# Performance work log

Measured on AMD Instinct MI355X. Metric: run time of the kernel, lower is better.

Reference implementation:

```python
import jax, jax.numpy as jnp
import numpy as np

B, S = 16, 32768
LEVELS = (5, 20)
TIME_DIM = 8
NUM_FREQS = 6  # frequency xyz encoder: 3*(1+2*6)=39 dims
HID = 128
IN_DIM = 3 * (1 + 2 * NUM_FREQS) + 2 * TIME_DIM  # 55


def setup_inputs() -> dict:
    key = jax.random.key(0)
    ks = jax.random.split(key, 16)
    time = jax.random.uniform(ks[0], (B,), dtype=jnp.float32)
    xyz = jax.random.uniform(ks[1], (B, S, 3), dtype=jnp.float32) * 2.0 - 1.0  # in [-1,1]
    te0 = jax.random.normal(ks[2], (LEVELS[0] + 1, TIME_DIM), dtype=jnp.float32)
    te1 = jax.random.normal(ks[3], (LEVELS[1] + 1, TIME_DIM), dtype=jnp.float32)
    W0 = jax.random.normal(ks[4], (IN_DIM, HID), dtype=jnp.float32) * 0.05
    b0 = jnp.zeros((HID,), dtype=jnp.float32)
    W1 = jax.random.normal(ks[5], (HID, HID), dtype=jnp.float32) * 0.05
    b1 = jnp.zeros((HID,), dtype=jnp.float32)
    W2 = jax.random.normal(ks[6], (HID, HID), dtype=jnp.float32) * 0.05
    b2 = jnp.zeros((HID,), dtype=jnp.float32)
    Wout = jax.random.normal(ks[7], (HID, 1), dtype=jnp.float32) * 0.05
    bout = jnp.zeros((1,), dtype=jnp.float32)
    return {"time": time, "xyz": xyz, "te0": te0, "te1": te1,
            "W0": W0, "b0": b0, "W1": W1, "b1": b1, "W2": W2, "b2": b2,
            "Wout": Wout, "bout": bout}


def _time_encode(t, emb, L):
    # bucketize t into L uniform intervals on [0,1), lerp between bucket endpoints
    tL = t * L
    idx = jnp.clip(jnp.floor(tL).astype(jnp.int32), 0, L - 1)  # (B,)
    w = (idx + 1).astype(t.dtype) - tL                          # weight for lower endpoint
    lerped = w[:, None] * emb[idx] + (1.0 - w)[:, None] * emb[idx + 1]
    # t >= 1: use last embedding directly (torch fallback branch)
    return jnp.where((t >= 1.0)[:, None], emb[L][None, :], lerped)


def _xyz_encode(x):
    # frequency encoding, include_input, freqs 2^0..2^(NUM_FREQS-1)
    freqs = jnp.asarray(2.0 ** np.arange(NUM_FREQS), dtype=x.dtype)  # (F,)
    xp = x[:, None, :] * freqs[None, :, None]                         # (N, F, 3)
    n = x.shape[0]
    return jnp.concatenate([x, jnp.sin(xp).reshape(n, -1), jnp.cos(xp).reshape(n, -1)], axis=-1)


def reference(time, xyz, te0, te1, W0, b0, W1, b1, W2, b2, Wout, bout):
    s = xyz.shape[1]
    t_enc = jnp.concatenate([_time_encode(time, te0, LEVELS[0]),
                             _time_encode(time, te1, LEVELS[1])], axis=-1)  # (B, 16)
    t_enc = jnp.repeat(t_enc, s, axis=0)          # (B*S, 16)  'B d -> (B S) d'
    pts = (xyz.reshape(-1, 3) + 1.0) / 2.0        # (B*S, 3)
    x = jnp.concatenate([t_enc, _xyz_encode(pts)], axis=1)  # (B*S, 55)
    x = jax.nn.relu(x @ W0 + b0)
    x = jax.nn.relu(x @ W1 + b1)
    x = jax.nn.relu(x @ W2 + b2)
    return x @ Wout + bout  # (B*S, 1)
```

## Files before the change

kernel.cpp:

```cpp
#include <hip/hip_runtime.h>

typedef _Float16 f16;
typedef __attribute__((ext_vector_type(2))) __fp16 fp16x2;
typedef __attribute__((ext_vector_type(8))) _Float16 f16x8;
typedef __attribute__((ext_vector_type(4))) float f32x4;
typedef __attribute__((ext_vector_type(4))) unsigned int u32x4;

#define NPTS   (16 * 32768)
#define W0P_OFF 0
#define W1P_OFF (16 * 1024)
#define W2P_OFF (48 * 1024)
#define WOP_OFF (80 * 1024)
#define FRAGS_BYTES (84 * 1024)
#define B0E_OFF FRAGS_BYTES
#define WS_NEEDED (FRAGS_BYTES + 8192)
#define LDS_TOTAL 4096

__global__ void pack_weights(const float* __restrict__ time, const float* __restrict__ te0,
                             const float* __restrict__ te1, const float* __restrict__ W0,
                             const float* __restrict__ b0, const float* __restrict__ W1,
                             const float* __restrict__ W2, const float* __restrict__ Wout,
                             unsigned char* __restrict__ ws) {
  const int bi = blockIdx.x;
  const int l = threadIdx.x;
  const int g = l >> 4, r16 = l & 15;
  if (bi < 84) {
    const float* W; int obase, fi, kt, mt, kmax; bool natural, outcol;
    if (bi < 16)      { W = W0;   fi = bi;      mt = fi >> 1; kt = fi & 1; obase = W0P_OFF; kmax = 39;  natural = true;  outcol = false; }
    else if (bi < 48) { W = W1;   fi = bi - 16; mt = fi >> 2; kt = fi & 3; obase = W1P_OFF; kmax = 128; natural = false; outcol = false; }
    else if (bi < 80) { W = W2;   fi = bi - 48; mt = fi >> 2; kt = fi & 3; obase = W2P_OFF; kmax = 128; natural = false; outcol = false; }
    else              { W = Wout; fi = bi - 80; mt = 0;       kt = fi;     obase = WOP_OFF; kmax = 128; natural = false; outcol = true;  }
    const int m = mt * 16 + r16;
    f16 vals[8] __attribute__((aligned(16)));
#pragma unroll
    for (int j = 0; j < 8; ++j) {
      const int k = natural ? (kt * 32 + g * 8 + j)
                            : (kt * 32 + (j >> 2) * 16 + g * 4 + (j & 3));
      float v = 0.f;
      if (k < kmax) {
        if (outcol)       v = (m == 0) ? Wout[k] : 0.f;
        else if (natural) v = W[(16 + k) * 128 + m];
        else              v = W[k * 128 + m];
      }
      vals[j] = (f16)v;
    }
    *(u32x4*)(ws + obase + (fi * 64 + l) * 16) = *(const u32x4*)vals;
  } else {
    const int idx = (bi - 84) * 64 + l;
    const int b = idx >> 7, m = idx & 127;
    const float t = time[b];
    float acc = b0[m];
#pragma unroll
    for (int d = 0; d < 16; ++d) {
      const float* emb; int L, dd;
      if (d < 8) { emb = te0; L = 5;  dd = d; }
      else       { emb = te1; L = 20; dd = d - 8; }
      const float tL = t * (float)L;
      int i = (int)floorf(tL);
      i = i < 0 ? 0 : (i > L - 1 ? L - 1 : i);
      const float wlo = (float)(i + 1) - tL;
      float v = wlo * emb[i * 8 + dd] + (1.f - wlo) * emb[(i + 1) * 8 + dd];
      if (t >= 1.f) v = emb[L * 8 + dd];
      acc += v * W0[d * 128 + m];
    }
    ((float*)(ws + B0E_OFF))[b * 128 + m] = acc;
  }
}

__device__ __forceinline__ unsigned int pkmax0(unsigned int x) {
  unsigned int r;
  asm("v_pk_max_f16 %0, %1, %2" : "=v"(r) : "v"(x), "v"(0u));
  return r;
}
__device__ __forceinline__ unsigned int pkrtz(float a, float b) {
  union { fp16x2 h; unsigned int u; } c;
  c.h = __builtin_amdgcn_cvt_pkrtz(a, b);
  return c.u;
}
__device__ __forceinline__ float hwsin_rev(float rev) {
  float r; asm("v_sin_f32 %0, %1" : "=v"(r) : "v"(rev)); return r;
}
__device__ __forceinline__ float hwcos_rev(float rev) {
  float r; asm("v_cos_f32 %0, %1" : "=v"(r) : "v"(rev)); return r;
}

template <int KT>
__device__ __forceinline__ void layer_swapped(const unsigned char* __restrict__ wsrc,
                                              const float* __restrict__ bias,
                                              const f16x8 (&Bin)[KT][4], f16x8 (&Bout)[4][4],
                                              int lane) {
  const int g4 = (lane >> 4) * 4;
  f16x8 Ab[2];
  Ab[0] = *(const f16x8*)(wsrc + (0 * 64 + lane) * 16);
#pragma unroll
  for (int mt = 0; mt < 8; ++mt) {
    const float4 bv = *(const float4*)(bias + mt * 16 + g4);
    f32x4 acc[4];
#pragma unroll
    for (int nt = 0; nt < 4; ++nt) acc[nt] = (f32x4){bv.x, bv.y, bv.z, bv.w};
#pragma unroll
    for (int kt = 0; kt < KT; ++kt) {
      const int s = mt * KT + kt;
      if (s + 1 < 8 * KT)
        Ab[(s + 1) & 1] = *(const f16x8*)(wsrc + ((s + 1) * 64 + lane) * 16);
      __builtin_amdgcn_s_setprio(1);
#pragma unroll
      for (int nt = 0; nt < 4; ++nt)
        acc[nt] = __builtin_amdgcn_mfma_f32_16x16x32_f16(Ab[s & 1], Bin[kt][nt], acc[nt], 0, 0, 0);
      __builtin_amdgcn_s_setprio(0);
    }
#pragma unroll
    for (int nt = 0; nt < 4; ++nt) {
      union { f16x8 v; unsigned int w[4]; } ub;
      ub.v = Bout[mt >> 1][nt];
      ub.w[2 * (mt & 1) + 0] = pkmax0(pkrtz(acc[nt][0], acc[nt][1]));
      ub.w[2 * (mt & 1) + 1] = pkmax0(pkrtz(acc[nt][2], acc[nt][3]));
      Bout[mt >> 1][nt] = ub.v;
    }
  }
}

__global__ void __launch_bounds__(64, 1)
mlp_main(const float* __restrict__ xyz, const float* __restrict__ b1,
         const float* __restrict__ b2, const float* __restrict__ bout,
         const unsigned char* __restrict__ ws, float* __restrict__ out) {
  extern __shared__ char lds[];
  const int lane = threadIdx.x;
  const int g = lane >> 4, r16 = lane & 15;

  char* scr = lds;
  const float bo = bout[0];

  const int pbase = blockIdx.x * 64;
  const int p = pbase + lane;

  float ff[40];
  const float xs0 = xyz[p * 3], xs1 = xyz[p * 3 + 1], xs2 = xyz[p * 3 + 2];
  const float pcs[3] = {(xs0 + 1.f) * 0.5f, (xs1 + 1.f) * 0.5f, (xs2 + 1.f) * 0.5f};
  const float INV2PI = 0.15915494309189535f;
#pragma unroll
  for (int c = 0; c < 3; ++c) {
    ff[c] = pcs[c];
    const float rev = pcs[c] * INV2PI;
    float s = hwsin_rev(rev), co = hwcos_rev(rev);
#pragma unroll
    for (int f = 0; f < 6; ++f) {
      ff[3 + f * 3 + c] = s;
      ff[21 + f * 3 + c] = co;
      const float s2 = 2.f * s * co, c2 = 1.f - 2.f * s * s;
      s = s2; co = c2;
    }
  }
  ff[39] = 0.f;
  unsigned int fw[32];
#pragma unroll
  for (int i = 0; i < 20; ++i) fw[i] = pkrtz(ff[2 * i], ff[2 * i + 1]);
#pragma unroll
  for (int i = 20; i < 32; ++i) fw[i] = 0u;

  f16x8 B0[2][4];
#pragma unroll
  for (int h = 0; h < 2; ++h) {
    if ((lane >> 5) == h) {
#pragma unroll
      for (int s = 0; s < 8; ++s)
        *(u32x4*)(scr + (lane & 31) * 128 + ((s ^ (lane & 7)) * 16)) = ((const u32x4*)fw)[s];
    }
    asm volatile("s_waitcnt lgkmcnt(0)" ::: "memory");
#pragma unroll
    for (int kt = 0; kt < 2; ++kt)
#pragma unroll
      for (int nn = 0; nn < 2; ++nn) {
        const int row = nn * 16 + r16;
        B0[kt][h * 2 + nn] = *(const f16x8*)(scr + row * 128 + (((4 * kt + g) ^ (row & 7)) * 16));
      }
    asm volatile("s_waitcnt lgkmcnt(0)" ::: "memory");
  }

  const float* b0e = (const float*)(ws + B0E_OFF) + (blockIdx.x >> 9) * 128;
  f16x8 Bx[4][4], By[4][4];
  layer_swapped<2>(ws + W0P_OFF, b0e, B0, Bx, lane);
  layer_swapped<4>(ws + W1P_OFF, b1, Bx, By, lane);
  layer_swapped<4>(ws + W2P_OFF, b2, By, Bx, lane);

  f16x8 Ob[2];
  Ob[0] = *(const f16x8*)(ws + WOP_OFF + (0 * 64 + lane) * 16);
  const f32x4 bovec = (f32x4){bo, bo, bo, bo};
  f32x4 accO[4];
#pragma unroll
  for (int kt = 0; kt < 4; ++kt) {
    if (kt + 1 < 4)
      Ob[(kt + 1) & 1] = *(const f16x8*)(ws + WOP_OFF + ((kt + 1) * 64 + lane) * 16);
    __builtin_amdgcn_s_setprio(1);
    if (kt == 0) {
#pragma unroll
      for (int nt = 0; nt < 4; ++nt)
        accO[nt] = __builtin_amdgcn_mfma_f32_16x16x32_f16(Ob[0], Bx[0][nt], bovec, 0, 0, 0);
    } else {
#pragma unroll
      for (int nt = 0; nt < 4; ++nt)
        accO[nt] = __builtin_amdgcn_mfma_f32_16x16x32_f16(Ob[kt & 1], Bx[kt][nt], accO[nt], 0, 0, 0);
    }
    __builtin_amdgcn_s_setprio(0);
  }

  const float a0 = __shfl(accO[0][0], r16, 64);
  const float a1 = __shfl(accO[1][0], r16, 64);
  const float a2 = __shfl(accO[2][0], r16, 64);
  const float a3 = __shfl(accO[3][0], r16, 64);
  const float v = g == 0 ? a0 : g == 1 ? a1 : g == 2 ? a2 : a3;
  out[pbase + lane] = v;
}

extern "C" void kernel_launch(void* const* d_in, const int* in_sizes, int n_in,
                              void* d_out, int out_size, void* d_ws, size_t ws_size,
                              hipStream_t stream) {
  const float* time = (const float*)d_in[0];
  const float* xyz  = (const float*)d_in[1];
  const float* te0  = (const float*)d_in[2];
  const float* te1  = (const float*)d_in[3];
  const float* W0   = (const float*)d_in[4];
  const float* b0   = (const float*)d_in[5];
  const float* W1   = (const float*)d_in[6];
  const float* b1   = (const float*)d_in[7];
  const float* W2   = (const float*)d_in[8];
  const float* b2   = (const float*)d_in[9];
  const float* Wout = (const float*)d_in[10];
  const float* bout = (const float*)d_in[11];
  float* out = (float*)d_out;
  unsigned char* ws = (unsigned char*)d_ws;
  if (ws_size < WS_NEEDED) return;

  pack_weights<<<116, 64, 0, stream>>>(time, te0, te1, W0, b0, W1, W2, Wout, ws);
  mlp_main<<<NPTS / 64, 64, LDS_TOTAL, stream>>>(xyz, b1, b2, bout, ws, out);
}
```

Measured before the change: 48.31 us.

## Process 96 points per wave and fold time encoding into layer-0 input

Each single-wave block now handles 96 points (6 N-tiles) instead of 64, so every weight fragment load feeds more MFMAs. The per-batch layer-0 bias folding is replaced by putting the 16 time-encoding features into the first-layer input (K=55 within two K-tiles), which simplifies pack_weights and builds features twice per wave. Launch bounds are relaxed to allow 2 waves per SIMD. The cost is more registers for the wider accumulators and activations, which risks spills or lower occupancy, plus a tail block with clamped indices.

```diff
diff --git a/kernel.cpp b/kernel.cpp
--- a/kernel.cpp
+++ b/kernel.cpp
@@ -7,63 +7,57 @@
 typedef __attribute__((ext_vector_type(4))) unsigned int u32x4;
 
 #define NPTS   (16 * 32768)
+#define PTSPB  96
+#define NBLK   ((NPTS + PTSPB - 1) / PTSPB)
 #define W0P_OFF 0
 #define W1P_OFF (16 * 1024)
 #define W2P_OFF (48 * 1024)
 #define WOP_OFF (80 * 1024)
 #define FRAGS_BYTES (84 * 1024)
-#define B0E_OFF FRAGS_BYTES
-#define WS_NEEDED (FRAGS_BYTES + 8192)
+#define TENC_OFF FRAGS_BYTES
+#define WS_NEEDED (FRAGS_BYTES + 1024)
 #define LDS_TOTAL 4096
 
 __global__ void pack_weights(const float* __restrict__ time, const float* __restrict__ te0,
                              const float* __restrict__ te1, const float* __restrict__ W0,
-                             const float* __restrict__ b0, const float* __restrict__ W1,
-                             const float* __restrict__ W2, const float* __restrict__ Wout,
-                             unsigned char* __restrict__ ws) {
+                             const float* __restrict__ W1, const float* __restrict__ W2,
+                             const float* __restrict__ Wout, unsigned char* __restrict__ ws) {
   const int bi = blockIdx.x;
   const int l = threadIdx.x;
   const int g = l >> 4, r16 = l & 15;
   if (bi < 84) {
     const float* W; int obase, fi, kt, mt, kmax; bool natural, outcol;
-    if (bi < 16)      { W = W0;   fi = bi;      mt = fi >> 1; kt = fi & 1; obase = W0P_OFF; kmax = 39;  natural = true;  outcol = false; }
+    if (bi < 16)      { W = W0;   fi = bi;      mt = fi >> 1; kt = fi & 1; obase = W0P_OFF; kmax = 55;  natural = true;  outcol = false; }
     else if (bi < 48) { W = W1;   fi = bi - 16; mt = fi >> 2; kt = fi & 3; obase = W1P_OFF; kmax = 128; natural = false; outcol = false; }
     else if (bi < 80) { W = W2;   fi = bi - 48; mt = fi >> 2; kt = fi & 3; obase = W2P_OFF; kmax = 128; natural = false; outcol = false; }
     else              { W = Wout; fi = bi - 80; mt = 0;       kt = fi;     obase = WOP_OFF; kmax = 128; natural = false; outcol = true;  }
     const int m = mt * 16 + r16;
+    int KTl = (bi < 16) ? 2 : 4;
+    int si = outcol ? kt : (mt * KTl + kt);
     f16 vals[8] __attribute__((aligned(16)));
 #pragma unroll
     for (int j = 0; j < 8; ++j) {
       const int k = natural ? (kt * 32 + g * 8 + j)
                             : (kt * 32 + (j >> 2) * 16 + g * 4 + (j & 3));
       float v = 0.f;
-      if (k < kmax) {
-        if (outcol)       v = (m == 0) ? Wout[k] : 0.f;
-        else if (natural) v = W[(16 + k) * 128 + m];
-        else              v = W[k * 128 + m];
-      }
+      if (k < kmax) v = outcol ? ((m == 0) ? Wout[k] : 0.f) : W[k * 128 + m];
       vals[j] = (f16)v;
     }
-    *(u32x4*)(ws + obase + (fi * 64 + l) * 16) = *(const u32x4*)vals;
+    *(u32x4*)(ws + obase + (si * 64 + l) * 16) = *(const u32x4*)vals;
   } else {
     const int idx = (bi - 84) * 64 + l;
-    const int b = idx >> 7, m = idx & 127;
+    const int b = idx >> 4, d = idx & 15;
     const float t = time[b];
-    float acc = b0[m];
-#pragma unroll
-    for (int d = 0; d < 16; ++d) {
-      const float* emb; int L, dd;
-      if (d < 8) { emb = te0; L = 5;  dd = d; }
-      else       { emb = te1; L = 20; dd = d - 8; }
-      const float tL = t * (float)L;
-      int i = (int)floorf(tL);
-      i = i < 0 ? 0 : (i > L - 1 ? L - 1 : i);
-      const float wlo = (float)(i + 1) - tL;
-      float v = wlo * emb[i * 8 + dd] + (1.f - wlo) * emb[(i + 1) * 8 + dd];
-      if (t >= 1.f) v = emb[L * 8 + dd];
-      acc += v * W0[d * 128 + m];
-    }
-    ((float*)(ws + B0E_OFF))[b * 128 + m] = acc;
+    const float* emb; int L, dd;
+    if (d < 8) { emb = te0; L = 5;  dd = d; }
+    else       { emb = te1; L = 20; dd = d - 8; }
+    const float tL = t * (float)L;
+    int i = (int)floorf(tL);
+    i = i < 0 ? 0 : (i > L - 1 ? L - 1 : i);
+    const float wlo = (float)(i + 1) - tL;
+    float v = wlo * emb[i * 8 + dd] + (1.f - wlo) * emb[(i + 1) * 8 + dd];
+    if (t >= 1.f) v = emb[L * 8 + dd];
+    ((float*)(ws + TENC_OFF))[idx] = v;
   }
 }
 
@@ -84,10 +78,38 @@
   float r; asm("v_cos_f32 %0, %1" : "=v"(r) : "v"(rev)); return r;
 }
 
+__device__ __forceinline__ void build_feat(const float* __restrict__ xyz,
+                                           const unsigned char* __restrict__ ws,
+                                           int p, unsigned int* fw) {
+  const float* tb = (const float*)(ws + TENC_OFF) + (p >> 15) * 16;
+  float ff[64];
+#pragma unroll
+  for (int i = 0; i < 16; ++i) ff[i] = tb[i];
+  const float xs0 = xyz[p * 3], xs1 = xyz[p * 3 + 1], xs2 = xyz[p * 3 + 2];
+  const float pcs[3] = {(xs0 + 1.f) * 0.5f, (xs1 + 1.f) * 0.5f, (xs2 + 1.f) * 0.5f};
+  const float INV2PI = 0.15915494309189535f;
+#pragma unroll
+  for (int c = 0; c < 3; ++c) {
+    ff[16 + c] = pcs[c];
+    float s = hwsin_rev(pcs[c] * INV2PI), co = hwcos_rev(pcs[c] * INV2PI);
+#pragma unroll
+    for (int f = 0; f < 6; ++f) {
+      ff[19 + f * 3 + c] = s;
+      ff[37 + f * 3 + c] = co;
+      const float s2 = 2.f * s * co, c2 = 1.f - 2.f * s * s;
+      s = s2; co = c2;
+    }
+  }
+#pragma unroll
+  for (int i = 55; i < 64; ++i) ff[i] = 0.f;
+#pragma unroll
+  for (int i = 0; i < 32; ++i) fw[i] = pkrtz(ff[2 * i], ff[2 * i + 1]);
+}
+
 template <int KT>
 __device__ __forceinline__ void layer_swapped(const unsigned char* __restrict__ wsrc,
                                               const float* __restrict__ bias,
-                                              const f16x8 (&Bin)[KT][4], f16x8 (&Bout)[4][4],
+                                              const f16x8 (&Bin)[KT][6], f16x8 (&Bout)[4][6],
                                               int lane) {
   const int g4 = (lane >> 4) * 4;
   f16x8 Ab[2];
@@ -95,9 +117,9 @@
 #pragma unroll
   for (int mt = 0; mt < 8; ++mt) {
     const float4 bv = *(const float4*)(bias + mt * 16 + g4);
-    f32x4 acc[4];
-#pragma unroll
-    for (int nt = 0; nt < 4; ++nt) acc[nt] = (f32x4){bv.x, bv.y, bv.z, bv.w};
+    f32x4 acc[6];
+#pragma unroll
+    for (int nt = 0; nt < 6; ++nt) acc[nt] = (f32x4){bv.x, bv.y, bv.z, bv.w};
 #pragma unroll
     for (int kt = 0; kt < KT; ++kt) {
       const int s = mt * KT + kt;
@@ -105,12 +127,12 @@
         Ab[(s + 1) & 1] = *(const f16x8*)(wsrc + ((s + 1) * 64 + lane) * 16);
       __builtin_amdgcn_s_setprio(1);
 #pragma unroll
-      for (int nt = 0; nt < 4; ++nt)
+      for (int nt = 0; nt < 6; ++nt)
         acc[nt] = __builtin_amdgcn_mfma_f32_16x16x32_f16(Ab[s & 1], Bin[kt][nt], acc[nt], 0, 0, 0);
       __builtin_amdgcn_s_setprio(0);
     }
 #pragma unroll
-    for (int nt = 0; nt < 4; ++nt) {
+    for (int nt = 0; nt < 6; ++nt) {
       union { f16x8 v; unsigned int w[4]; } ub;
       ub.v = Bout[mt >> 1][nt];
       ub.w[2 * (mt & 1) + 0] = pkmax0(pkrtz(acc[nt][0], acc[nt][1]));
@@ -120,45 +142,25 @@
   }
 }
 
-__global__ void __launch_bounds__(64, 1)
-mlp_main(const float* __restrict__ xyz, const float* __restrict__ b1,
-         const float* __restrict__ b2, const float* __restrict__ bout,
-         const unsigned char* __restrict__ ws, float* __restrict__ out) {
+__global__ void __launch_bounds__(64, 2)
+mlp_main(const float* __restrict__ xyz, const float* __restrict__ b0,
+         const float* __restrict__ b1, const float* __restrict__ b2,
+         const float* __restrict__ bout, const unsigned char* __restrict__ ws,
+         float* __restrict__ out) {
   extern __shared__ char lds[];
   const int lane = threadIdx.x;
   const int g = lane >> 4, r16 = lane & 15;
-
   char* scr = lds;
   const float bo = bout[0];
 
-  const int pbase = blockIdx.x * 64;
-  const int p = pbase + lane;
-
-  float ff[40];
-  const float xs0 = xyz[p * 3], xs1 = xyz[p * 3 + 1], xs2 = xyz[p * 3 + 2];
-  const float pcs[3] = {(xs0 + 1.f) * 0.5f, (xs1 + 1.f) * 0.5f, (xs2 + 1.f) * 0.5f};
-  const float INV2PI = 0.15915494309189535f;
-#pragma unroll
-  for (int c = 0; c < 3; ++c) {
-    ff[c] = pcs[c];
-    const float rev = pcs[c] * INV2PI;
-    float s = hwsin_rev(rev), co = hwcos_rev(rev);
-#pragma unroll
-    for (int f = 0; f < 6; ++f) {
-      ff[3 + f * 3 + c] = s;
-      ff[21 + f * 3 + c] = co;
-      const float s2 = 2.f * s * co, c2 = 1.f - 2.f * s * s;
-      s = s2; co = c2;
-    }
-  }
-  ff[39] = 0.f;
+  const int pbase = blockIdx.x * PTSPB;
+
   unsigned int fw[32];
-#pragma unroll
-  for (int i = 0; i < 20; ++i) fw[i] = pkrtz(ff[2 * i], ff[2 * i + 1]);
-#pragma unroll
-  for (int i = 20; i < 32; ++i) fw[i] = 0u;
-
-  f16x8 B0[2][4];
+  {
+    int p = pbase + lane; p = p < NPTS ? p : NPTS - 1;
+    build_feat(xyz, ws, p, fw);
+  }
+  f16x8 B0[2][6];
 #pragma unroll
   for (int h = 0; h < 2; ++h) {
     if ((lane >> 5) == h) {
@@ -176,17 +178,34 @@
       }
     asm volatile("s_waitcnt lgkmcnt(0)" ::: "memory");
   }
-
-  const float* b0e = (const float*)(ws + B0E_OFF) + (blockIdx.x >> 9) * 128;
-  f16x8 Bx[4][4], By[4][4];
-  layer_swapped<2>(ws + W0P_OFF, b0e, B0, Bx, lane);
+  {
+    int p = pbase + 64 + (lane & 31); p = p < NPTS ? p : NPTS - 1;
+    build_feat(xyz, ws, p, fw);
+  }
+  if (lane < 32) {
+#pragma unroll
+    for (int s = 0; s < 8; ++s)
+      *(u32x4*)(scr + (lane & 31) * 128 + ((s ^ (lane & 7)) * 16)) = ((const u32x4*)fw)[s];
+  }
+  asm volatile("s_waitcnt lgkmcnt(0)" ::: "memory");
+#pragma unroll
+  for (int kt = 0; kt < 2; ++kt)
+#pragma unroll
+    for (int nn = 0; nn < 2; ++nn) {
+      const int row = nn * 16 + r16;
+      B0[kt][4 + nn] = *(const f16x8*)(scr + row * 128 + (((4 * kt + g) ^ (row & 7)) * 16));
+    }
+  asm volatile("s_waitcnt lgkmcnt(0)" ::: "memory");
+
+  f16x8 Bx[4][6], By[4][6];
+  layer_swapped<2>(ws + W0P_OFF, b0, B0, Bx, lane);
   layer_swapped<4>(ws + W1P_OFF, b1, Bx, By, lane);
   layer_swapped<4>(ws + W2P_OFF, b2, By, Bx, lane);
 
   f16x8 Ob[2];
   Ob[0] = *(const f16x8*)(ws + WOP_OFF + (0 * 64 + lane) * 16);
   const f32x4 bovec = (f32x4){bo, bo, bo, bo};
-  f32x4 accO[4];
+  f32x4 accO[6];
 #pragma unroll
   for (int kt = 0; kt < 4; ++kt) {
     if (kt + 1 < 4)
@@ -194,22 +213,31 @@
     __builtin_amdgcn_s_setprio(1);
     if (kt == 0) {
 #pragma unroll
-      for (int nt = 0; nt < 4; ++nt)
+      for (int nt = 0; nt < 6; ++nt)
         accO[nt] = __builtin_amdgcn_mfma_f32_16x16x32_f16(Ob[0], Bx[0][nt], bovec, 0, 0, 0);
     } else {
 #pragma unroll
-      for (int nt = 0; nt < 4; ++nt)
+      for (int nt = 0; nt < 6; ++nt)
         accO[nt] = __builtin_amdgcn_mfma_f32_16x16x32_f16(Ob[kt & 1], Bx[kt][nt], accO[nt], 0, 0, 0);
     }
     __builtin_amdgcn_s_setprio(0);
   }
 
-  const float a0 = __shfl(accO[0][0], r16, 64);
-  const float a1 = __shfl(accO[1][0], r16, 64);
-  const float a2 = __shfl(accO[2][0], r16, 64);
-  const float a3 = __shfl(accO[3][0], r16, 64);
-  const float v = g == 0 ? a0 : g == 1 ? a1 : g == 2 ? a2 : a3;
-  out[pbase + lane] = v;
+  {
+    const float a0 = __shfl(accO[0][0], r16, 64);
+    const float a1 = __shfl(accO[1][0], r16, 64);
+    const float a2 = __shfl(accO[2][0], r16, 64);
+    const float a3 = __shfl(accO[3][0], r16, 64);
+    const float v = g == 0 ? a0 : g == 1 ? a1 : g == 2 ? a2 : a3;
+    if (pbase + lane < NPTS) out[pbase + lane] = v;
+  }
+  {
+    const float a4 = __shfl(accO[4][0], r16, 64);
+    const float a5 = __shfl(accO[5][0], r16, 64);
+    const float v = ((lane >> 4) & 1) ? a5 : a4;
+    const int p = pbase + 64 + lane;
+    if (lane < 32 && p < NPTS) out[p] = v;
+  }
 }
 
 extern "C" void kernel_launch(void* const* d_in, const int* in_sizes, int n_in,
@@ -231,6 +259,6 @@
   unsigned char* ws = (unsigned char*)d_ws;
   if (ws_size < WS_NEEDED) return;
 
-  pack_weights<<<116, 64, 0, stream>>>(time, te0, te1, W0, b0, W1, W2, Wout, ws);
-  mlp_main<<<NPTS / 64, 64, LDS_TOTAL, stream>>>(xyz, b1, b2, bout, ws, out);
-}
+  pack_weights<<<88, 64, 0, stream>>>(time, te0, te1, W0, W1, W2, Wout, ws);
+  mlp_main<<<NBLK, 64, LDS_TOTAL, stream>>>(xyz, b0, b1, b2, bout, ws, out);
+}
```

Result: no change. 48.86 us (+1.1%).
